# Kernel optimization log

Measured on AMD Instinct MI355X. Metric: run time of the kernel, lower is better.

Reference implementation:

```python
import jax, jax.numpy as jnp
import numpy as np

DT = 0.05
TAU = 10.0
V_TH = 2.0
ALPHA = 1.0 - DT / TAU  # membrane leak factor (1 - dt/tau)


def setup_inputs() -> dict:
    key = jax.random.key(0)
    kx, kw = jax.random.split(key)
    B, T, N = 32, 1024, 2048
    x = jax.random.normal(kx, (B, T, N), dtype=jnp.float32)
    # w ~ Normal(0, 1/sqrt(N)) as in torch.nn.init.normal_(std=1/sqrt(N))
    w = jax.random.normal(kw, (N,), dtype=jnp.float32) * float(1.0 / np.sqrt(N))
    return {"x": x, "w": w}


def reference(x, w):
    """LIF recurrence with online eligibility-trace gradient, fused over time.

    Per step t (matching NeuronClass.__call__ then backward_online):
      v   = alpha*v + x_t @ w - v_th * z          (z from previous step, detached)
      z   = 1[v > v_th]
      eps = x_t - v * w                            # [B, N]
      g  += v * eps + (eps @ w) * p                # p is the PRE-update trace
      p   = alpha*p + x_t
    Returns (v_seq [B,T], z_seq [B,T], grad_acc [B,N]).
    """
    B, T, N = x.shape
    alpha = jnp.asarray(ALPHA, x.dtype)
    v_th = jnp.asarray(V_TH, x.dtype)
    xt = jnp.swapaxes(x, 0, 1)  # [T, B, N] for scan over time

    def step(carry, x_t):
        v, z, p, g = carry
        v = alpha * v + x_t @ w - v_th * z          # [B]
        z = (v > v_th).astype(x_t.dtype)            # hard threshold
        eps = x_t - v[:, None] * w                  # [B, N] prediction error
        g = g + v[:, None] * eps + (eps @ w)[:, None] * p
        p = alpha * p + x_t                         # trace updated AFTER use
        return (v, z, p, g), (v, z)

    v0 = jnp.zeros((B,), x.dtype)
    z0 = jnp.zeros((B,), x.dtype)
    p0 = jnp.zeros((B, N), x.dtype)
    g0 = jnp.zeros((B, N), x.dtype)
    (_, _, _, grad_acc), (v_seq, z_seq) = jax.lax.scan(step, (v0, z0, p0, g0), xt)
    return jnp.swapaxes(v_seq, 0, 1), jnp.swapaxes(z_seq, 0, 1), grad_acc
```

## Files before the change

### kernel.cpp

```cpp
#include <hip/hip_runtime.h>


#define ALPHA 0.995f
#define VTH   2.0f

constexpr int B = 32;
constexpr int T = 1024;
constexpr int N = 2048;
constexpr int TCH = 128;
constexpr int NTC = T / TCH;

typedef float floatx4 __attribute__((ext_vector_type(4)));

__device__ inline floatx4 ntload4(const float* p) {
    return __builtin_nontemporal_load(reinterpret_cast<const floatx4*>(p));
}

__global__ __launch_bounds__(256) void gemv_kernel(const float* __restrict__ x,
                                                   const float* __restrict__ w,
                                                   float* __restrict__ u) {
    const int wave = threadIdx.x >> 6;
    const int lane = threadIdx.x & 63;
    const int row0 = blockIdx.x * 16 + wave * 4;
    const float* xr = x + (size_t)row0 * N;
    float s0 = 0.f, s1 = 0.f, s2 = 0.f, s3 = 0.f;
#pragma unroll
    for (int k = 0; k < 8; ++k) {
        const int idx = k * 256 + lane * 4;
        const floatx4 wv = *reinterpret_cast<const floatx4*>(w + idx);
        const floatx4 a = ntload4(xr + idx);
        const floatx4 b = ntload4(xr + N + idx);
        const floatx4 c = ntload4(xr + 2 * N + idx);
        const floatx4 d = ntload4(xr + 3 * N + idx);
        s0 += a.x * wv.x + a.y * wv.y + a.z * wv.z + a.w * wv.w;
        s1 += b.x * wv.x + b.y * wv.y + b.z * wv.z + b.w * wv.w;
        s2 += c.x * wv.x + c.y * wv.y + c.z * wv.z + c.w * wv.w;
        s3 += d.x * wv.x + d.y * wv.y + d.z * wv.z + d.w * wv.w;
    }
#pragma unroll
    for (int off = 32; off; off >>= 1) {
        s0 += __shfl_down(s0, off);
        s1 += __shfl_down(s1, off);
        s2 += __shfl_down(s2, off);
        s3 += __shfl_down(s3, off);
    }
    if (lane == 0) {
        floatx4 r = {s0, s1, s2, s3};
        *reinterpret_cast<floatx4*>(u + row0) = r;
    }
}

__global__ __launch_bounds__(64) void scan_kernel(const float* __restrict__ w,
                                                  const float* __restrict__ u,
                                                  float* __restrict__ cbuf,
                                                  float* __restrict__ V2,
                                                  float* __restrict__ out_v,
                                                  float* __restrict__ out_z) {
    __shared__ float u_lds[T];
    __shared__ float v_lds[T];
    __shared__ float s_lds[T];
    __shared__ float c_lds[T];
    const int b    = blockIdx.x;
    const int lane = threadIdx.x;

    float wacc = 0.f;
#pragma unroll
    for (int i = 0; i < N / 64; ++i) {
        const float wv = w[i * 64 + lane];
        wacc += wv * wv;
    }
#pragma unroll
    for (int off = 32; off; off >>= 1) wacc += __shfl_xor(wacc, off);
    const float wsq = wacc;

#pragma unroll
    for (int k = 0; k < T / 256; ++k) {
        const int j = (k * 64 + lane) * 4;
        *reinterpret_cast<floatx4*>(&u_lds[j]) =
            *reinterpret_cast<const floatx4*>(&u[b * T + j]);
    }
    __syncthreads();

    if (lane == 0) {
        float v = 0.f, z = 0.f, v2 = 0.f;
        for (int cc = 0; cc < T / 32; ++cc) {
            const int base = cc * 32;
            floatx4 ub[8];
#pragma unroll
            for (int k = 0; k < 8; ++k)
                ub[k] = *reinterpret_cast<floatx4*>(&u_lds[base + k * 4]);
            floatx4 vb[8], sb[8];
#pragma unroll
            for (int k = 0; k < 8; ++k) {
#pragma unroll
                for (int e = 0; e < 4; ++e) {
                    const float ut = ub[k][e];
                    v = ALPHA * v + ut - VTH * z;
                    z = (v > VTH) ? 1.f : 0.f;
                    vb[k][e] = v;
                    sb[k][e] = ut - v * wsq;
                    v2 += v * v;
                }
            }
#pragma unroll
            for (int k = 0; k < 8; ++k) {
                *reinterpret_cast<floatx4*>(&v_lds[base + k * 4]) = vb[k];
                *reinterpret_cast<floatx4*>(&s_lds[base + k * 4]) = sb[k];
            }
        }
        V2[b] = v2;
        float q = 0.f;
        for (int cc = T / 32 - 1; cc >= 0; --cc) {
            const int base = cc * 32;
            floatx4 sb[8], vb[8], cb[8];
#pragma unroll
            for (int k = 0; k < 8; ++k) {
                sb[k] = *reinterpret_cast<floatx4*>(&s_lds[base + k * 4]);
                vb[k] = *reinterpret_cast<floatx4*>(&v_lds[base + k * 4]);
            }
#pragma unroll
            for (int k = 7; k >= 0; --k) {
#pragma unroll
                for (int e = 3; e >= 0; --e) {
                    cb[k][e] = vb[k][e] + q;
                    q = sb[k][e] + ALPHA * q;
                }
            }
#pragma unroll
            for (int k = 0; k < 8; ++k)
                *reinterpret_cast<floatx4*>(&c_lds[base + k * 4]) = cb[k];
        }
    }
    __syncthreads();

#pragma unroll
    for (int k = 0; k < T / 256; ++k) {
        const int j = (k * 64 + lane) * 4;
        const floatx4 vv = *reinterpret_cast<floatx4*>(&v_lds[j]);
        floatx4 zz;
        zz.x = (vv.x > VTH) ? 1.f : 0.f;
        zz.y = (vv.y > VTH) ? 1.f : 0.f;
        zz.z = (vv.z > VTH) ? 1.f : 0.f;
        zz.w = (vv.w > VTH) ? 1.f : 0.f;
        *reinterpret_cast<floatx4*>(&out_v[b * T + j]) = vv;
        *reinterpret_cast<floatx4*>(&out_z[b * T + j]) = zz;
        *reinterpret_cast<floatx4*>(&cbuf[b * T + j]) =
            *reinterpret_cast<floatx4*>(&c_lds[j]);
    }
}

__global__ __launch_bounds__(256) void accum_kernel(const float* __restrict__ x,
                                                    const float* __restrict__ c,
                                                    float* __restrict__ gpart) {
    __shared__ float cs[TCH];
    const int b   = blockIdx.z;
    const int nc  = blockIdx.y;
    const int tc  = blockIdx.x;
    const int t0  = tc * TCH;
    const int tid = threadIdx.x;
    if (tid < TCH) cs[tid] = c[b * T + t0 + tid];
    __syncthreads();

    const int n = nc * 1024 + tid * 4;
    const float* xb = x + ((size_t)b * T + t0) * N + n;
    floatx4 acc = {0.f, 0.f, 0.f, 0.f};
#pragma unroll 8
    for (int tt = 0; tt < TCH; ++tt) {
        const floatx4 xv = ntload4(xb + (size_t)tt * N);
        const float cc = cs[tt];
        acc.x += cc * xv.x;
        acc.y += cc * xv.y;
        acc.z += cc * xv.z;
        acc.w += cc * xv.w;
    }
    *reinterpret_cast<floatx4*>(gpart + ((size_t)tc * B + b) * N + n) = acc;
}

__global__ __launch_bounds__(256) void reduce_kernel(const float* __restrict__ gpart,
                                                     const float* __restrict__ w,
                                                     const float* __restrict__ V2,
                                                     float* __restrict__ g) {
    const int i = blockIdx.x * 256 + threadIdx.x;
    const int b = i >> 11;
    const int n = i & (N - 1);
    float acc = -V2[b] * w[n];
#pragma unroll
    for (int tc = 0; tc < NTC; ++tc) acc += gpart[tc * (B * N) + i];
    g[i] = acc;
}

extern "C" void kernel_launch(void* const* d_in, const int* in_sizes, int n_in,
                              void* d_out, int out_size, void* d_ws, size_t ws_size,
                              hipStream_t stream) {
    const float* x = (const float*)d_in[0];
    const float* w = (const float*)d_in[1];

    float* out   = (float*)d_out;
    float* out_v = out;
    float* out_z = out + B * T;
    float* out_g = out + 2 * B * T;

    float* u     = (float*)d_ws;
    float* c     = u + B * T;
    float* V2    = c + B * T;
    float* gpart = V2 + B;

    gemv_kernel<<<(B * T) / 16, 256, 0, stream>>>(x, w, u);
    scan_kernel<<<B, 64, 0, stream>>>(w, u, c, V2, out_v, out_z);
    accum_kernel<<<dim3(NTC, N / 1024, B), 256, 0, stream>>>(x, c, gpart);
    reduce_kernel<<<(B * N) / 256, 256, 0, stream>>>(gpart, w, V2, out_g);
}
```

Before: 411.9 us.

## Reverse accum traversal order to reuse cached x tail from gemv pass

Replaces nontemporal loads of x with regular loads in both the gemv and accum passes. The accum kernel now walks batches, time chunks and timesteps in reverse, so it starts on the end of x that the gemv pass touched last and may still sit in L2 or the MALL/Infinity Cache. Outputs are written with nontemporal stores so they do not evict that cached data. The benefit is bounded by cache size relative to the 256MB input, and regular loads could pollute the cache during the streaming passes.

```diff
diff --git a/kernel.cpp b/kernel.cpp
--- a/kernel.cpp
+++ b/kernel.cpp
@@ -12,8 +12,11 @@
 
 typedef float floatx4 __attribute__((ext_vector_type(4)));
 
-__device__ inline floatx4 ntload4(const float* p) {
-    return __builtin_nontemporal_load(reinterpret_cast<const floatx4*>(p));
+__device__ inline floatx4 load4(const float* p) {
+    return *reinterpret_cast<const floatx4*>(p);
+}
+__device__ inline void ntstore4(float* p, floatx4 v) {
+    __builtin_nontemporal_store(v, reinterpret_cast<floatx4*>(p));
 }
 
 __global__ __launch_bounds__(256) void gemv_kernel(const float* __restrict__ x,
@@ -27,11 +30,11 @@
 #pragma unroll
     for (int k = 0; k < 8; ++k) {
         const int idx = k * 256 + lane * 4;
-        const floatx4 wv = *reinterpret_cast<const floatx4*>(w + idx);
-        const floatx4 a = ntload4(xr + idx);
-        const floatx4 b = ntload4(xr + N + idx);
-        const floatx4 c = ntload4(xr + 2 * N + idx);
-        const floatx4 d = ntload4(xr + 3 * N + idx);
+        const floatx4 wv = load4(w + idx);
+        const floatx4 a = load4(xr + idx);
+        const floatx4 b = load4(xr + N + idx);
+        const floatx4 c = load4(xr + 2 * N + idx);
+        const floatx4 d = load4(xr + 3 * N + idx);
         s0 += a.x * wv.x + a.y * wv.y + a.z * wv.z + a.w * wv.w;
         s1 += b.x * wv.x + b.y * wv.y + b.z * wv.z + b.w * wv.w;
         s2 += c.x * wv.x + c.y * wv.y + c.z * wv.z + c.w * wv.w;
@@ -76,8 +79,7 @@
 #pragma unroll
     for (int k = 0; k < T / 256; ++k) {
         const int j = (k * 64 + lane) * 4;
-        *reinterpret_cast<floatx4*>(&u_lds[j]) =
-            *reinterpret_cast<const floatx4*>(&u[b * T + j]);
+        *reinterpret_cast<floatx4*>(&u_lds[j]) = load4(&u[b * T + j]);
     }
     __syncthreads();
 
@@ -142,8 +144,8 @@
         zz.y = (vv.y > VTH) ? 1.f : 0.f;
         zz.z = (vv.z > VTH) ? 1.f : 0.f;
         zz.w = (vv.w > VTH) ? 1.f : 0.f;
-        *reinterpret_cast<floatx4*>(&out_v[b * T + j]) = vv;
-        *reinterpret_cast<floatx4*>(&out_z[b * T + j]) = zz;
+        ntstore4(&out_v[b * T + j], vv);
+        ntstore4(&out_z[b * T + j], zz);
         *reinterpret_cast<floatx4*>(&cbuf[b * T + j]) =
             *reinterpret_cast<floatx4*>(&c_lds[j]);
     }
@@ -153,9 +155,9 @@
                                                     const float* __restrict__ c,
                                                     float* __restrict__ gpart) {
     __shared__ float cs[TCH];
-    const int b   = blockIdx.z;
+    const int b   = (B - 1) - blockIdx.z;
     const int nc  = blockIdx.y;
-    const int tc  = blockIdx.x;
+    const int tc  = (NTC - 1) - blockIdx.x;
     const int t0  = tc * TCH;
     const int tid = threadIdx.x;
     if (tid < TCH) cs[tid] = c[b * T + t0 + tid];
@@ -165,8 +167,8 @@
     const float* xb = x + ((size_t)b * T + t0) * N + n;
     floatx4 acc = {0.f, 0.f, 0.f, 0.f};
 #pragma unroll 8
-    for (int tt = 0; tt < TCH; ++tt) {
-        const floatx4 xv = ntload4(xb + (size_t)tt * N);
+    for (int tt = TCH - 1; tt >= 0; --tt) {
+        const floatx4 xv = load4(xb + (size_t)tt * N);
         const float cc = cs[tt];
         acc.x += cc * xv.x;
         acc.y += cc * xv.y;
@@ -186,7 +188,7 @@
     float acc = -V2[b] * w[n];
 #pragma unroll
     for (int tc = 0; tc < NTC; ++tc) acc += gpart[tc * (B * N) + i];
-    g[i] = acc;
+    __builtin_nontemporal_store(acc, &g[i]);
 }
 
 extern "C" void kernel_launch(void* const* d_in, const int* in_sizes, int n_in,
```

Measured after the change: 432.0 us. 1.05x slower.
